# Optimization experiments

Measured on AMD Instinct MI355X. Metric: run time of the kernel, lower is better.

The kernel has to match this reference:

```python
import jax, jax.numpy as jnp
import numpy as np
from math import sqrt

H = 16  # head_num


def setup_inputs() -> dict:
    key = jax.random.key(0)
    ks = jax.random.split(key, 8)
    B, Sq, Skv, Dq, Dkv, Dall = 2, 2048, 2048, 1024, 1024, 1024
    x = jax.random.normal(ks[0], (B, Sq, Dq), dtype=jnp.float32)
    y = jax.random.normal(ks[1], (B, Skv, Dkv), dtype=jnp.float32)
    attention_mask = jnp.ones((B, 1, Sq, Skv), dtype=jnp.int32)
    # torch nn.Linear weights are [out, in]
    Wq = jax.random.normal(ks[2], (Dall, Dq), dtype=jnp.float32) * 0.02
    Wk = jax.random.normal(ks[3], (Dall, Dkv), dtype=jnp.float32) * 0.02
    Wv = jax.random.normal(ks[4], (Dall, Dkv), dtype=jnp.float32) * 0.02
    Wo = jax.random.normal(ks[5], (Dq, Dall), dtype=jnp.float32) * 0.02
    bo = jnp.zeros((Dq,), dtype=jnp.float32)
    return {"x": x, "y": y, "attention_mask": attention_mask,
            "Wq": Wq, "Wk": Wk, "Wv": Wv, "Wo": Wo, "bo": bo}


def reference(x, y, attention_mask, Wq, Wk, Wv, Wo, bo):
    B, Sq, _ = x.shape
    Dall = Wq.shape[0]
    Dh = Dall // H
    # projections (torch Linear: x @ W.T), split heads -> [B, H, S, Dh]
    q = (x @ Wq.T).reshape(B, Sq, H, Dh).transpose(0, 2, 1, 3)
    k = (y @ Wk.T).reshape(B, -1, H, Dh).transpose(0, 2, 1, 3)
    v = (y @ Wv.T).reshape(B, -1, H, Dh).transpose(0, 2, 1, 3)
    scores = jnp.einsum('bhqd,bhkd->bhqk', q, k)  # [B,H,Sq,Skv]
    mask = (attention_mask == 0)  # masked_fill where mask.eq(0) -> but torch does mask.eq(0) then fills True positions
    scores = jnp.where(mask, jnp.float32(-1e9), scores)
    # NOTE: faithful quirk - mask applied before scaling; scale uses sqrt(h_size)
    attn = jax.nn.softmax(scores / sqrt(Dh), axis=-1)
    out = jnp.einsum('bhqk,bhkd->bhqd', attn, v)
    out = out.transpose(0, 2, 1, 3).reshape(B, Sq, Dall)
    return out @ Wo.T + bo
```

## Files before the change

kernel.cpp:

```cpp
#include <hip/hip_runtime.h>
#include <stdint.h>


typedef __attribute__((ext_vector_type(8))) short bf16x8;
typedef __attribute__((ext_vector_type(4))) float f32x4;
typedef __attribute__((ext_vector_type(16))) float f32x16;
typedef __attribute__((ext_vector_type(2))) unsigned int u32x2;

#define LOG2E 1.44269504088896f

static __device__ __forceinline__ unsigned short f2bf(float f) {
  union { float f; unsigned int u; } v; v.f = f;
  unsigned int r = v.u + 0x7FFFu + ((v.u >> 16) & 1u);
  return (unsigned short)(r >> 16);
}

static __device__ __forceinline__ void g2l16(const void* gsrc, void* ldst) {
  __builtin_amdgcn_global_load_lds((const __attribute__((address_space(1))) unsigned int*)gsrc,
                                   (__attribute__((address_space(3))) unsigned int*)ldst,
                                   16, 0, 0);
}

static __device__ __forceinline__ unsigned int cvt_pk_bf16(float lo, float hi) {
  unsigned int r;
  asm("v_cvt_pk_bf16_f32 %0, %1, %2" : "=v"(r) : "v"(lo), "v"(hi));
  return r;
}

static __device__ __forceinline__ u32x2 pl32swap(unsigned int a, unsigned int b) {
  return __builtin_amdgcn_permlane32_swap(a, b, false, false);
}

static __device__ __forceinline__ f32x16 mfma32(bf16x8 a, bf16x8 b, f32x16 c) {
  return __builtin_amdgcn_mfma_f32_32x32x16_bf16(a, b, c, 0, 0, 0);
}

static __device__ __forceinline__ size_t kfrag_addr(int row, int col) {
  int b = row >> 11, s = row & 2047;
  int h = col >> 6, d = col & 63;
  int t32 = s >> 5, r31 = s & 31;
  int ks = d >> 4, r5 = (d >> 3) & 1, e = d & 7;
  return (size_t)(b * 16 + h) * 131072 + (size_t)t32 * 2048 + ks * 512 + (r5 * 32 + r31) * 8 + e;
}
static __device__ __forceinline__ size_t vfrag_addr(int row, int col) {
  int b = row >> 11, s = row & 2047;
  int h = col >> 6, d = col & 63;
  int t64 = s >> 6, k2 = (s >> 4) & 3, r5 = (s >> 3) & 1, e = s & 7;
  int mb = d >> 5, r31 = d & 31;
  return (size_t)(b * 16 + h) * 131072 + (size_t)t64 * 4096 + (mb * 4 + k2) * 512 + (r5 * 32 + r31) * 8 + e;
}

__global__ void k_cvt2(const float* __restrict__ a, const float* __restrict__ b,
                       unsigned short* __restrict__ oa, unsigned short* __restrict__ ob, int n) {
  const float* in = blockIdx.y ? b : a;
  unsigned short* out = blockIdx.y ? ob : oa;
  int i = (blockIdx.x * blockDim.x + threadIdx.x) * 4;
  int stride = gridDim.x * blockDim.x * 4;
  for (; i < n; i += stride) {
    float4 v = *reinterpret_cast<const float4*>(in + i);
    ushort4 o;
    o.x = f2bf(v.x); o.y = f2bf(v.y); o.z = f2bf(v.z); o.w = f2bf(v.w);
    *reinterpret_cast<ushort4*>(out + i) = o;
  }
}

__global__ void k_cvt4(const float* __restrict__ a, const float* __restrict__ b,
                       const float* __restrict__ c, const float* __restrict__ d,
                       unsigned short* __restrict__ oa, unsigned short* __restrict__ ob,
                       unsigned short* __restrict__ oc, unsigned short* __restrict__ od, int n) {
  const float* in; unsigned short* out;
  switch (blockIdx.y) {
    case 0: in = a; out = oa; break;
    case 1: in = b; out = ob; break;
    case 2: in = c; out = oc; break;
    default: in = d; out = od; break;
  }
  int i = (blockIdx.x * blockDim.x + threadIdx.x) * 4;
  int stride = gridDim.x * blockDim.x * 4;
  for (; i < n; i += stride) {
    float4 v = *reinterpret_cast<const float4*>(in + i);
    ushort4 o;
    o.x = f2bf(v.x); o.y = f2bf(v.y); o.z = f2bf(v.z); o.w = f2bf(v.w);
    *reinterpret_cast<ushort4*>(out + i) = o;
  }
}

__global__ void k_pack_mask(const int* __restrict__ mask, unsigned long long* __restrict__ bits,
                            unsigned int* __restrict__ flag) {
  size_t gw = (size_t)blockIdx.x * 4 + (threadIdx.x >> 6);
  int lane = threadIdx.x & 63;
  int m = mask[gw * 64 + lane];
  unsigned long long bal = __ballot(m != 0);
  if (lane == 0) {
    bits[gw] = bal;
    if (bal != ~0ull) atomicAnd(flag, 0u);
  }
}

template <int OM>
static __device__ __forceinline__ void gemm_body(const unsigned short* __restrict__ A,
                                                 const unsigned short* __restrict__ W,
                                                 void* __restrict__ Cout,
                                                 const float* __restrict__ bias) {
  __shared__ __align__(16) unsigned short As[128 * 32];
  __shared__ __align__(16) unsigned short Bs[128 * 32];
  const int tid = threadIdx.x;
  const int w = tid >> 6, lane = tid & 63;
  const int wr = w >> 1, wc = w & 1;
  const int l15 = lane & 15, lg = lane >> 4;
  const int bm = blockIdx.x, bn = blockIdx.y;

  f32x4 acc[4][4] = {};

  const int e0 = w * 1024 + lane * 8;
  const int e1 = e0 + 512;
  const int r0 = e0 >> 5, c0 = e0 & 31;
  const int r1 = e1 >> 5, c1 = e1 & 31;
  const unsigned short* A0 = A + (size_t)(bm * 128 + r0) * 1024 + c0;
  const unsigned short* A1 = A + (size_t)(bm * 128 + r1) * 1024 + c1;
  const unsigned short* W0 = W + (size_t)(bn * 128 + r0) * 1024 + c0;
  const unsigned short* W1 = W + (size_t)(bn * 128 + r1) * 1024 + c1;

  for (int kt = 0; kt < 1024; kt += 32) {
    g2l16(A0 + kt, (char*)As + e0 * 2);
    g2l16(A1 + kt, (char*)As + e1 * 2);
    g2l16(W0 + kt, (char*)Bs + e0 * 2);
    g2l16(W1 + kt, (char*)Bs + e1 * 2);
    __syncthreads();
    bf16x8 a[4], b[4];
#pragma unroll
    for (int mi = 0; mi < 4; ++mi)
      a[mi] = *reinterpret_cast<const bf16x8*>(As + (wr * 64 + mi * 16 + l15) * 32 + lg * 8);
#pragma unroll
    for (int ni = 0; ni < 4; ++ni)
      b[ni] = *reinterpret_cast<const bf16x8*>(Bs + (wc * 64 + ni * 16 + l15) * 32 + lg * 8);
#pragma unroll
    for (int mi = 0; mi < 4; ++mi)
#pragma unroll
      for (int ni = 0; ni < 4; ++ni)
        acc[mi][ni] = __builtin_amdgcn_mfma_f32_16x16x32_bf16(a[mi], b[ni], acc[mi][ni], 0, 0, 0);
    __syncthreads();
  }

#pragma unroll
  for (int ni = 0; ni < 4; ++ni) {
    const int gcol = bn * 128 + wc * 64 + ni * 16 + l15;
    float bv = (OM == 1) ? bias[gcol] : 0.f;
#pragma unroll
    for (int mi = 0; mi < 4; ++mi) {
#pragma unroll
      for (int r = 0; r < 4; ++r) {
        const int grow = bm * 128 + wr * 64 + mi * 16 + lg * 4 + r;
        if (OM == 0)
          ((unsigned short*)Cout)[(size_t)grow * 1024 + gcol] = f2bf(acc[mi][ni][r]);
        else if (OM == 1)
          ((float*)Cout)[(size_t)grow * 1024 + gcol] = acc[mi][ni][r] + bv;
        else if (OM == 2)
          ((unsigned short*)Cout)[kfrag_addr(grow, gcol)] = f2bf(acc[mi][ni][r]);
        else
          ((unsigned short*)Cout)[vfrag_addr(grow, gcol)] = f2bf(acc[mi][ni][r]);
      }
    }
  }
}

__global__ __launch_bounds__(256) void k_gemm_qkv(
    const unsigned short* __restrict__ xb, const unsigned short* __restrict__ yb,
    const unsigned short* __restrict__ Wq, const unsigned short* __restrict__ Wk,
    const unsigned short* __restrict__ Wv,
    unsigned short* __restrict__ Qf, unsigned short* __restrict__ Kf,
    unsigned short* __restrict__ Vf) {
  const int z = blockIdx.z;
  if (z == 0) gemm_body<2>(xb, Wq, Qf, nullptr);
  else if (z == 1) gemm_body<2>(yb, Wk, Kf, nullptr);
  else gemm_body<3>(yb, Wv, Vf, nullptr);
}

__global__ __launch_bounds__(256) void k_gemm_o(
    const unsigned short* __restrict__ AO, const unsigned short* __restrict__ Wo,
    float* __restrict__ out, const float* __restrict__ bo) {
  gemm_body<1>(AO, Wo, out, bo);
}


#define BUILD_PB2(SP, K2, IDX) {                                   \
    unsigned int c0_ = cvt_pk_bf16(SP[(K2)*8 + 0], SP[(K2)*8 + 1]);\
    unsigned int c1_ = cvt_pk_bf16(SP[(K2)*8 + 2], SP[(K2)*8 + 3]);\
    unsigned int c2_ = cvt_pk_bf16(SP[(K2)*8 + 4], SP[(K2)*8 + 5]);\
    unsigned int c3_ = cvt_pk_bf16(SP[(K2)*8 + 6], SP[(K2)*8 + 7]);\
    u32x2 r0_ = pl32swap(c0_, c2_);                                \
    u32x2 r1_ = pl32swap(c1_, c3_);                                \
    union { unsigned int u[4]; bf16x8 v; } f_;                     \
    f_.u[0] = r0_.x; f_.u[1] = r1_.x; f_.u[2] = r0_.y; f_.u[3] = r1_.y; \
    pb[IDX] = f_.v; }

#define STAGE_TILE(T, BUF) {                                                  \
    const size_t toff_ = (size_t)(T) * 8192;                                  \
    char* kb_ = smem + (BUF) * 16384;                                         \
    const int o0_ = (w * 2 + 0) * 1024 + lane * 16;                           \
    const int o1_ = (w * 2 + 1) * 1024 + lane * 16;                           \
    g2l16(Kg + toff_ + o0_, kb_ + o0_);                                       \
    g2l16(Kg + toff_ + o1_, kb_ + o1_);                                       \
    g2l16(Vg + toff_ + o0_, kb_ + 8192 + o0_);                                \
    g2l16(Vg + toff_ + o1_, kb_ + 8192 + o1_);                                \
  }

__global__ __launch_bounds__(256, 2) void k_attn(
    const unsigned short* __restrict__ Qf, const unsigned short* __restrict__ Kf,
    const unsigned short* __restrict__ Vf, const unsigned long long* __restrict__ bits,
    const unsigned int* __restrict__ flag, unsigned short* __restrict__ AO) {
  __shared__ __align__(16) char smem[32768];
  const int tid = threadIdx.x, w = tid >> 6, lane = tid & 63;
  const int l31 = lane & 31, hi = lane >> 5;
  const int bid = blockIdx.x;
  const int xcd = bid & 7, rr = bid >> 3;
  const int j = rr & 15;
  const int g = xcd + ((rr >> 4) << 3);
  const int h = g & 15, b = g >> 4;
  const int q = j * 128 + w * 32 + l31;
  const bool allfull = (*flag == 0xFFFFFFFFu);
  const float C1 = 0.125f * LOG2E;
  const f32x16 z16 = {};

  const size_t bh = (size_t)(b * 16 + h) * 131072;
  bf16x8 qf[4];
  const unsigned short* Qp = Qf + bh + (size_t)(j * 4 + w) * 2048 + lane * 8;
#pragma unroll
  for (int ks = 0; ks < 4; ++ks)
    qf[ks] = *reinterpret_cast<const bf16x8*>(Qp + ks * 512);

  const char* Kg = (const char*)(Kf + bh);
  const char* Vg = (const char*)(Vf + bh);
  const unsigned long long* brow = bits + (size_t)(b * 2048 + q) * 32;

  f32x16 o0 = {}, o1 = {};
  float m_run = -3e38f, l_run = 0.f;

  STAGE_TILE(0, 0)
  __syncthreads();

  for (int t = 0; t < 32; ++t) {
    const int cur = t & 1;
    if (t < 31) STAGE_TILE(t + 1, cur ^ 1)
    const char* Kb = smem + cur * 16384;
    const char* Vb = Kb + 8192;

    bf16x8 kf[8], vf[8];
#pragma unroll
    for (int f = 0; f < 8; ++f)
      kf[f] = *reinterpret_cast<const bf16x8*>(Kb + f * 1024 + lane * 16);

    f32x16 s0 = z16, s1 = z16;
#pragma unroll
    for (int ks = 0; ks < 4; ++ks) {
      s0 = mfma32(kf[ks], qf[ks], s0);
      s1 = mfma32(kf[4 + ks], qf[ks], s1);
    }

#pragma unroll
    for (int f = 0; f < 8; ++f)
      vf[f] = *reinterpret_cast<const bf16x8*>(Vb + f * 1024 + lane * 16);

    if (!allfull) {
      unsigned long long wb = brow[t];
      if (!__all(wb == ~0ull)) {
#pragma unroll
        for (int r = 0; r < 16; ++r) {
          const int kl = (r & 3) + 8 * (r >> 2) + 4 * hi;
          s0[r] = ((wb >> kl) & 1ull) ? s0[r] : -1e9f;
          s1[r] = ((wb >> (kl + 32)) & 1ull) ? s1[r] : -1e9f;
        }
      }
    }

    float mx[8];
#pragma unroll
    for (int r = 0; r < 8; ++r)
      mx[r] = fmaxf(fmaxf(s0[r], s0[r + 8]), fmaxf(s1[r], s1[r + 8]));
    mx[0] = fmaxf(mx[0], mx[4]); mx[1] = fmaxf(mx[1], mx[5]);
    mx[2] = fmaxf(mx[2], mx[6]); mx[3] = fmaxf(mx[3], mx[7]);
    mx[0] = fmaxf(mx[0], mx[2]); mx[1] = fmaxf(mx[1], mx[3]);
    float tm = fmaxf(mx[0], mx[1]);
    {
      u32x2 sw = pl32swap(__builtin_bit_cast(unsigned int, tm),
                          __builtin_bit_cast(unsigned int, tm));
      tm = fmaxf(__builtin_bit_cast(float, sw.x), __builtin_bit_cast(float, sw.y));
    }
    tm *= 0.125f;

    if (__any(tm > m_run + 8.f)) {
      const float mn = fmaxf(m_run, tm);
      const float al = __builtin_amdgcn_exp2f((m_run - mn) * LOG2E);
      m_run = mn; l_run *= al;
#pragma unroll
      for (int r = 0; r < 16; ++r) { o0[r] *= al; o1[r] *= al; }
    }

    const float mc = m_run * LOG2E;
    float ls;
#pragma unroll
    for (int r = 0; r < 16; ++r) {
      s0[r] = __builtin_amdgcn_exp2f(s0[r] * C1 - mc);
      s1[r] = __builtin_amdgcn_exp2f(s1[r] * C1 - mc);
    }
    {
      float sm[8];
#pragma unroll
      for (int r = 0; r < 8; ++r) sm[r] = (s0[r] + s0[r + 8]) + (s1[r] + s1[r + 8]);
      sm[0] += sm[4]; sm[1] += sm[5]; sm[2] += sm[6]; sm[3] += sm[7];
      sm[0] += sm[2]; sm[1] += sm[3];
      ls = sm[0] + sm[1];
      u32x2 sw = pl32swap(__builtin_bit_cast(unsigned int, ls),
                          __builtin_bit_cast(unsigned int, ls));
      ls = __builtin_bit_cast(float, sw.x) + __builtin_bit_cast(float, sw.y);
    }
    l_run += ls;

    bf16x8 pb[4];
    BUILD_PB2(s0, 0, 0) BUILD_PB2(s0, 1, 1) BUILD_PB2(s1, 0, 2) BUILD_PB2(s1, 1, 3)
#pragma unroll
    for (int k2 = 0; k2 < 4; ++k2) {
      o0 = mfma32(vf[k2], pb[k2], o0);
      o1 = mfma32(vf[4 + k2], pb[k2], o1);
    }
    __syncthreads();
  }

  const float inv = 1.f / l_run;
  unsigned short* Orow = AO + (size_t)(b * 2048 + q) * 1024 + h * 64;
#pragma unroll
  for (int g2 = 0; g2 < 4; ++g2) {
    ushort4 pk;
    pk.x = f2bf(o0[g2 * 4 + 0] * inv);
    pk.y = f2bf(o0[g2 * 4 + 1] * inv);
    pk.z = f2bf(o0[g2 * 4 + 2] * inv);
    pk.w = f2bf(o0[g2 * 4 + 3] * inv);
    *reinterpret_cast<ushort4*>(Orow + 8 * g2 + 4 * hi) = pk;
    pk.x = f2bf(o1[g2 * 4 + 0] * inv);
    pk.y = f2bf(o1[g2 * 4 + 1] * inv);
    pk.z = f2bf(o1[g2 * 4 + 2] * inv);
    pk.w = f2bf(o1[g2 * 4 + 3] * inv);
    *reinterpret_cast<ushort4*>(Orow + 32 + 8 * g2 + 4 * hi) = pk;
  }
}

extern "C" void kernel_launch(void* const* d_in, const int* in_sizes, int n_in,
                              void* d_out, int out_size, void* d_ws, size_t ws_size,
                              hipStream_t stream) {
  const float* x  = (const float*)d_in[0];
  const float* y  = (const float*)d_in[1];
  const int* mask = (const int*)d_in[2];
  const float* Wq = (const float*)d_in[3];
  const float* Wk = (const float*)d_in[4];
  const float* Wv = (const float*)d_in[5];
  const float* Wo = (const float*)d_in[6];
  const float* bo = (const float*)d_in[7];

  char* ws = (char*)d_ws;
  const size_t MB = 1ull << 20;
  unsigned short* xb  = (unsigned short*)(ws + 0 * MB);
  unsigned short* yb  = (unsigned short*)(ws + 8 * MB);
  unsigned short* Wqb = (unsigned short*)(ws + 16 * MB);
  unsigned short* Wkb = (unsigned short*)(ws + 18 * MB);
  unsigned short* Wvb = (unsigned short*)(ws + 20 * MB);
  unsigned short* Wob = (unsigned short*)(ws + 22 * MB);
  unsigned short* Qf  = (unsigned short*)(ws + 24 * MB);
  unsigned short* Kf  = (unsigned short*)(ws + 32 * MB);
  unsigned short* Vf  = (unsigned short*)(ws + 40 * MB);
  unsigned short* AOb = (unsigned short*)(ws + 56 * MB);
  unsigned long long* bits = (unsigned long long*)(ws + 64 * MB);
  unsigned int* flag = (unsigned int*)(ws + 65 * MB);

  hipMemsetAsync(flag, 0xFF, 4, stream);
  k_cvt2<<<dim3(2048, 2), 256, 0, stream>>>(x, y, xb, yb, 4194304);
  k_cvt4<<<dim3(512, 4), 256, 0, stream>>>(Wq, Wk, Wv, Wo, Wqb, Wkb, Wvb, Wob, 1048576);
  k_pack_mask<<<32768, 256, 0, stream>>>(mask, bits, flag);
  k_gemm_qkv<<<dim3(32, 8, 3), 256, 0, stream>>>(xb, yb, Wqb, Wkb, Wvb, Qf, Kf, Vf);
  k_attn<<<512, 256, 0, stream>>>(Qf, Kf, Vf, bits, flag, AOb);
  k_gemm_o<<<dim3(32, 8, 1), 256, 0, stream>>>(AOb, Wob, (float*)d_out, bo);
}
```

Baseline: 140.9 us.

## Split attention KV range across wave pairs and fuse prep kernels

The three preprocessing kernels (activation cast, weight cast, mask packing) are merged into one launch, and the mask packer now issues one atomic per warp instead of one per word. The attention kernel now handles 64 queries per block instead of 128, and the four waves split into two query halves times two KV halves (split-K flash attention). The partial softmax states are merged through shared memory at the end. This doubles the attention grid to 1024 blocks for better occupancy and load balance. In exchange the KV double-buffered prefetch is removed, so each iteration loads then syncs without overlap, and a cross-wave reduction is added.

```diff
diff --git a/kernel.cpp b/kernel.cpp
--- a/kernel.cpp
+++ b/kernel.cpp
@@ -50,50 +50,46 @@
   return (size_t)(b * 16 + h) * 131072 + (size_t)t64 * 4096 + (mb * 4 + k2) * 512 + (r5 * 32 + r31) * 8 + e;
 }
 
-__global__ void k_cvt2(const float* __restrict__ a, const float* __restrict__ b,
-                       unsigned short* __restrict__ oa, unsigned short* __restrict__ ob, int n) {
-  const float* in = blockIdx.y ? b : a;
-  unsigned short* out = blockIdx.y ? ob : oa;
+__global__ void k_prep(const float* __restrict__ x, const float* __restrict__ y,
+                       const float* __restrict__ Wq, const float* __restrict__ Wk,
+                       const float* __restrict__ Wv, const float* __restrict__ Wo,
+                       const int* __restrict__ mask,
+                       unsigned short* __restrict__ xb, unsigned short* __restrict__ yb,
+                       unsigned short* __restrict__ Wqb, unsigned short* __restrict__ Wkb,
+                       unsigned short* __restrict__ Wvb, unsigned short* __restrict__ Wob,
+                       unsigned long long* __restrict__ bits, unsigned int* __restrict__ flag) {
+  const int task = blockIdx.y;
+  if (task == 6) {
+    const int lane = threadIdx.x & 63;
+    int gw = blockIdx.x * 4 + (threadIdx.x >> 6);
+    bool any0 = false;
+    for (; gw < 131072; gw += 4096) {
+      int m = mask[(size_t)gw * 64 + lane];
+      unsigned long long bal = __ballot(m != 0);
+      if (lane == 0) {
+        bits[gw] = bal;
+        any0 |= (bal != ~0ull);
+      }
+    }
+    if (lane == 0 && any0) atomicAnd(flag, 0u);
+    return;
+  }
+  const float* in; unsigned short* out; int n;
+  switch (task) {
+    case 0: in = x;  out = xb;  n = 4194304; break;
+    case 1: in = y;  out = yb;  n = 4194304; break;
+    case 2: in = Wq; out = Wqb; n = 1048576; break;
+    case 3: in = Wk; out = Wkb; n = 1048576; break;
+    case 4: in = Wv; out = Wvb; n = 1048576; break;
+    default: in = Wo; out = Wob; n = 1048576; break;
+  }
   int i = (blockIdx.x * blockDim.x + threadIdx.x) * 4;
-  int stride = gridDim.x * blockDim.x * 4;
+  const int stride = gridDim.x * blockDim.x * 4;
   for (; i < n; i += stride) {
     float4 v = *reinterpret_cast<const float4*>(in + i);
     ushort4 o;
     o.x = f2bf(v.x); o.y = f2bf(v.y); o.z = f2bf(v.z); o.w = f2bf(v.w);
     *reinterpret_cast<ushort4*>(out + i) = o;
-  }
-}
-
-__global__ void k_cvt4(const float* __restrict__ a, const float* __restrict__ b,
-                       const float* __restrict__ c, const float* __restrict__ d,
-                       unsigned short* __restrict__ oa, unsigned short* __restrict__ ob,
-                       unsigned short* __restrict__ oc, unsigned short* __restrict__ od, int n) {
-  const float* in; unsigned short* out;
-  switch (blockIdx.y) {
-    case 0: in = a; out = oa; break;
-    case 1: in = b; out = ob; break;
-    case 2: in = c; out = oc; break;
-    default: in = d; out = od; break;
-  }
-  int i = (blockIdx.x * blockDim.x + threadIdx.x) * 4;
-  int stride = gridDim.x * blockDim.x * 4;
-  for (; i < n; i += stride) {
-    float4 v = *reinterpret_cast<const float4*>(in + i);
-    ushort4 o;
-    o.x = f2bf(v.x); o.y = f2bf(v.y); o.z = f2bf(v.z); o.w = f2bf(v.w);
-    *reinterpret_cast<ushort4*>(out + i) = o;
-  }
-}
-
-__global__ void k_pack_mask(const int* __restrict__ mask, unsigned long long* __restrict__ bits,
-                            unsigned int* __restrict__ flag) {
-  size_t gw = (size_t)blockIdx.x * 4 + (threadIdx.x >> 6);
-  int lane = threadIdx.x & 63;
-  int m = mask[gw * 64 + lane];
-  unsigned long long bal = __ballot(m != 0);
-  if (lane == 0) {
-    bits[gw] = bal;
-    if (bal != ~0ull) atomicAnd(flag, 0u);
   }
 }
 
@@ -194,17 +190,6 @@
     f_.u[0] = r0_.x; f_.u[1] = r1_.x; f_.u[2] = r0_.y; f_.u[3] = r1_.y; \
     pb[IDX] = f_.v; }
 
-#define STAGE_TILE(T, BUF) {                                                  \
-    const size_t toff_ = (size_t)(T) * 8192;                                  \
-    char* kb_ = smem + (BUF) * 16384;                                         \
-    const int o0_ = (w * 2 + 0) * 1024 + lane * 16;                           \
-    const int o1_ = (w * 2 + 1) * 1024 + lane * 16;                           \
-    g2l16(Kg + toff_ + o0_, kb_ + o0_);                                       \
-    g2l16(Kg + toff_ + o1_, kb_ + o1_);                                       \
-    g2l16(Vg + toff_ + o0_, kb_ + 8192 + o0_);                                \
-    g2l16(Vg + toff_ + o1_, kb_ + 8192 + o1_);                                \
-  }
-
 __global__ __launch_bounds__(256, 2) void k_attn(
     const unsigned short* __restrict__ Qf, const unsigned short* __restrict__ Kf,
     const unsigned short* __restrict__ Vf, const unsigned long long* __restrict__ bits,
@@ -212,19 +197,20 @@
   __shared__ __align__(16) char smem[32768];
   const int tid = threadIdx.x, w = tid >> 6, lane = tid & 63;
   const int l31 = lane & 31, hi = lane >> 5;
+  const int sq = w & 1, kvh = w >> 1;
   const int bid = blockIdx.x;
   const int xcd = bid & 7, rr = bid >> 3;
-  const int j = rr & 15;
-  const int g = xcd + ((rr >> 4) << 3);
+  const int jj = rr & 31;
+  const int g = xcd + ((rr >> 5) << 3);
   const int h = g & 15, b = g >> 4;
-  const int q = j * 128 + w * 32 + l31;
+  const int q = jj * 64 + sq * 32 + l31;
   const bool allfull = (*flag == 0xFFFFFFFFu);
   const float C1 = 0.125f * LOG2E;
   const f32x16 z16 = {};
 
   const size_t bh = (size_t)(b * 16 + h) * 131072;
   bf16x8 qf[4];
-  const unsigned short* Qp = Qf + bh + (size_t)(j * 4 + w) * 2048 + lane * 8;
+  const unsigned short* Qp = Qf + bh + (size_t)(jj * 2 + sq) * 2048 + lane * 8;
 #pragma unroll
   for (int ks = 0; ks < 4; ++ks)
     qf[ks] = *reinterpret_cast<const bf16x8*>(Qp + ks * 512);
@@ -235,15 +221,24 @@
 
   f32x16 o0 = {}, o1 = {};
   float m_run = -3e38f, l_run = 0.f;
-
-  STAGE_TILE(0, 0)
-  __syncthreads();
-
-  for (int t = 0; t < 32; ++t) {
-    const int cur = t & 1;
-    if (t < 31) STAGE_TILE(t + 1, cur ^ 1)
-    const char* Kb = smem + cur * 16384;
-    const char* Vb = Kb + 8192;
+  const int t0 = kvh * 16;
+  const char* Kb = smem + kvh * 16384;
+  const char* Vb = Kb + 8192;
+  const int lo = tid * 16;
+
+  for (int i = 0; i < 16; ++i) {
+    {
+      const size_t a = (size_t)i * 8192, c = (size_t)(16 + i) * 8192;
+      g2l16(Kg + a + lo,        smem + lo);
+      g2l16(Kg + a + 4096 + lo, smem + 4096 + lo);
+      g2l16(Vg + a + lo,        smem + 8192 + lo);
+      g2l16(Vg + a + 4096 + lo, smem + 12288 + lo);
+      g2l16(Kg + c + lo,        smem + 16384 + lo);
+      g2l16(Kg + c + 4096 + lo, smem + 20480 + lo);
+      g2l16(Vg + c + lo,        smem + 24576 + lo);
+      g2l16(Vg + c + 4096 + lo, smem + 28672 + lo);
+    }
+    __syncthreads();
 
     bf16x8 kf[8], vf[8];
 #pragma unroll
@@ -262,7 +257,7 @@
       vf[f] = *reinterpret_cast<const bf16x8*>(Vb + f * 1024 + lane * 16);
 
     if (!allfull) {
-      unsigned long long wb = brow[t];
+      unsigned long long wb = brow[t0 + i];
       if (!__all(wb == ~0ull)) {
 #pragma unroll
         for (int r = 0; r < 16; ++r) {
@@ -326,21 +321,41 @@
     __syncthreads();
   }
 
-  const float inv = 1.f / l_run;
-  unsigned short* Orow = AO + (size_t)(b * 2048 + q) * 1024 + h * 64;
-#pragma unroll
-  for (int g2 = 0; g2 < 4; ++g2) {
-    ushort4 pk;
-    pk.x = f2bf(o0[g2 * 4 + 0] * inv);
-    pk.y = f2bf(o0[g2 * 4 + 1] * inv);
-    pk.z = f2bf(o0[g2 * 4 + 2] * inv);
-    pk.w = f2bf(o0[g2 * 4 + 3] * inv);
-    *reinterpret_cast<ushort4*>(Orow + 8 * g2 + 4 * hi) = pk;
-    pk.x = f2bf(o1[g2 * 4 + 0] * inv);
-    pk.y = f2bf(o1[g2 * 4 + 1] * inv);
-    pk.z = f2bf(o1[g2 * 4 + 2] * inv);
-    pk.w = f2bf(o1[g2 * 4 + 3] * inv);
-    *reinterpret_cast<ushort4*>(Orow + 32 + 8 * g2 + 4 * hi) = pk;
+  float* LoF = (float*)smem;
+  float* LmlF = (float*)(smem + 16384);
+  if (kvh == 1) {
+#pragma unroll
+    for (int r = 0; r < 16; ++r) {
+      LoF[(sq * 32 + r) * 64 + lane] = o0[r];
+      LoF[(sq * 32 + 16 + r) * 64 + lane] = o1[r];
+    }
+    LmlF[sq * 128 + lane] = m_run;
+    LmlF[sq * 128 + 64 + lane] = l_run;
+  }
+  __syncthreads();
+  if (kvh == 0) {
+    const float m_b = LmlF[sq * 128 + lane];
+    const float l_b = LmlF[sq * 128 + 64 + lane];
+    const float mn = fmaxf(m_run, m_b);
+    const float aa = __builtin_amdgcn_exp2f((m_run - mn) * LOG2E);
+    const float ab = __builtin_amdgcn_exp2f((m_b - mn) * LOG2E);
+    const float linv = 1.f / (l_run * aa + l_b * ab);
+    const float fa = aa * linv, fb = ab * linv;
+    unsigned short* Orow = AO + (size_t)(b * 2048 + q) * 1024 + h * 64;
+#pragma unroll
+    for (int g2 = 0; g2 < 4; ++g2) {
+      ushort4 pk;
+      pk.x = f2bf(o0[g2 * 4 + 0] * fa + LoF[(sq * 32 + g2 * 4 + 0) * 64 + lane] * fb);
+      pk.y = f2bf(o0[g2 * 4 + 1] * fa + LoF[(sq * 32 + g2 * 4 + 1) * 64 + lane] * fb);
+      pk.z = f2bf(o0[g2 * 4 + 2] * fa + LoF[(sq * 32 + g2 * 4 + 2) * 64 + lane] * fb);
+      pk.w = f2bf(o0[g2 * 4 + 3] * fa + LoF[(sq * 32 + g2 * 4 + 3) * 64 + lane] * fb);
+      *reinterpret_cast<ushort4*>(Orow + 8 * g2 + 4 * hi) = pk;
+      pk.x = f2bf(o1[g2 * 4 + 0] * fa + LoF[(sq * 32 + 16 + g2 * 4 + 0) * 64 + lane] * fb);
+      pk.y = f2bf(o1[g2 * 4 + 1] * fa + LoF[(sq * 32 + 16 + g2 * 4 + 1) * 64 + lane] * fb);
+      pk.z = f2bf(o1[g2 * 4 + 2] * fa + LoF[(sq * 32 + 16 + g2 * 4 + 2) * 64 + lane] * fb);
+      pk.w = f2bf(o1[g2 * 4 + 3] * fa + LoF[(sq * 32 + 16 + g2 * 4 + 3) * 64 + lane] * fb);
+      *reinterpret_cast<ushort4*>(Orow + 32 + 8 * g2 + 4 * hi) = pk;
+    }
   }
 }
 
@@ -372,10 +387,9 @@
   unsigned int* flag = (unsigned int*)(ws + 65 * MB);
 
   hipMemsetAsync(flag, 0xFF, 4, stream);
-  k_cvt2<<<dim3(2048, 2), 256, 0, stream>>>(x, y, xb, yb, 4194304);
-  k_cvt4<<<dim3(512, 4), 256, 0, stream>>>(Wq, Wk, Wv, Wo, Wqb, Wkb, Wvb, Wob, 1048576);
-  k_pack_mask<<<32768, 256, 0, stream>>>(mask, bits, flag);
+  k_prep<<<dim3(1024, 7), 256, 0, stream>>>(x, y, Wq, Wk, Wv, Wo, mask,
+                                            xb, yb, Wqb, Wkb, Wvb, Wob, bits, flag);
   k_gemm_qkv<<<dim3(32, 8, 3), 256, 0, stream>>>(xb, yb, Wqb, Wkb, Wvb, Qf, Kf, Vf);
-  k_attn<<<512, 256, 0, stream>>>(Qf, Kf, Vf, bits, flag, AOb);
+  k_attn<<<1024, 256, 0, stream>>>(Qf, Kf, Vf, bits, flag, AOb);
   k_gemm_o<<<dim3(32, 8, 1), 256, 0, stream>>>(AOb, Wob, (float*)d_out, bo);
 }
```

Measured after the change: 142.2 us. About the same (+0.9%).
